# Performance work log

Hardware: AMD Instinct MI355X
Metric: run time of the kernel (lower is better)

Reference implementation:

```python
import jax, jax.numpy as jnp
import numpy as np

N_BINS = 4  # default meteorological bins: [0,5), [5,25), [25,50), [50,100) mm/h in log1p scale


def setup_inputs() -> dict:
    key = jax.random.key(0)
    k1, k2, k3 = jax.random.split(key, 3)
    shape = (16, 1, 15, 384, 384)
    # y_true in [0, 5) (log1p scale) so that all precipitation bins are populated
    y_true = jax.random.uniform(k1, shape, dtype=jnp.float32) * 5.0
    # y_pred: prediction = truth + noise, stays near truth like a trained model
    y_pred = y_true + 0.5 * jax.random.normal(k2, shape, dtype=jnp.float32)
    return {"y_pred": y_pred, "y_true": y_true}


def reference(y_pred, y_true):
    # bins = log1p([0, 5, 25, 50, 100])
    bins = jnp.log1p(jnp.array([0.0, 5.0, 25.0, 50.0, 100.0], dtype=y_true.dtype))
    yp = y_pred.reshape(-1)
    yt = y_true.reshape(-1)
    # bin index i such that bins[i] <= yt < bins[i+1]; -1 below, N_BINS at/above top
    idx = jnp.digitize(yt, bins) - 1
    valid = (idx >= 0) & (idx < N_BINS)
    seg = jnp.where(valid, idx, N_BINS)  # route out-of-range values to a dump bin
    sq = (yp - yt) ** 2
    sumsq = jax.ops.segment_sum(jnp.where(valid, sq, 0.0), seg, num_segments=N_BINS + 1)[:N_BINS]
    counts = jax.ops.segment_sum(valid.astype(yt.dtype), seg, num_segments=N_BINS + 1)[:N_BINS]
    present = counts > 0
    csafe = jnp.where(present, counts, 1.0)
    mse = sumsq / csafe                              # per-bin MSE (0 for empty bins)
    w = jnp.where(present, 1.0 / csafe, 0.0)         # inverse-frequency weights
    wsum = jnp.sum(w)
    wn = w / jnp.where(wsum > 0, wsum, 1.0)          # normalized over non-empty bins
    weighted_mse = jnp.sum(wn * mse)
    loss = jnp.sqrt(weighted_mse + 1e-8)
    return jnp.where(jnp.any(present), loss, jnp.zeros_like(loss))
```

## Files before the change

kernel.cpp:

```cpp
#include <hip/hip_runtime.h>
#include <math.h>

#define NBINS 4
#define SLOTS 64
#define UNROLL 4


__global__ __launch_bounds__(256) void qrmse_bins(
    const float4* __restrict__ yp4, const float4* __restrict__ yt4,
    const float* __restrict__ yp, const float* __restrict__ yt,
    float* __restrict__ g_ss, unsigned int* __restrict__ g_cnt,
    int n4, int n)
{
    const float B1 = 1.7917594909667969f;
    const float B2 = 3.2580965518951416f;
    const float B3 = 3.9318256378173828f;
    const float B4 = 4.6151204109191895f;

    float ss0 = 0.f, ss1 = 0.f, ss2 = 0.f, ss3 = 0.f;
    unsigned int c0 = 0, c1 = 0, c2 = 0, c3 = 0;

    const int base = blockIdx.x * (blockDim.x * UNROLL) + threadIdx.x;

    float4 p[UNROLL], t[UNROLL];
#pragma unroll
    for (int k = 0; k < UNROLL; ++k) {
        int idx = base + k * 256;
        if (idx < n4) {
            p[k] = yp4[idx];
            t[k] = yt4[idx];
        } else {
            p[k] = make_float4(0.f, 0.f, 0.f, 0.f);
            t[k] = make_float4(-1.f, -1.f, -1.f, -1.f);
        }
    }

#define ACC(PC, TC)                                          \
    {                                                        \
        float d  = (PC) - (TC);                              \
        float sq = d * d;                                    \
        float tv = (TC);                                     \
        bool b0 = (tv >= 0.f) & (tv < B1);                   \
        bool b1 = (tv >= B1)  & (tv < B2);                   \
        bool b2 = (tv >= B2)  & (tv < B3);                   \
        bool b3 = (tv >= B3)  & (tv < B4);                   \
        ss0 += b0 ? sq : 0.f;  c0 += b0;                     \
        ss1 += b1 ? sq : 0.f;  c1 += b1;                     \
        ss2 += b2 ? sq : 0.f;  c2 += b2;                     \
        ss3 += b3 ? sq : 0.f;  c3 += b3;                     \
    }

#pragma unroll
    for (int k = 0; k < UNROLL; ++k) {
        ACC(p[k].x, t[k].x); ACC(p[k].y, t[k].y);
        ACC(p[k].z, t[k].z); ACC(p[k].w, t[k].w);
    }

    if (blockIdx.x == 0 && threadIdx.x == 0) {
        for (int i = n4 * 4; i < n; ++i) {
            float pp = yp[i];
            float tt = yt[i];
            ACC(pp, tt);
        }
    }
#undef ACC

    for (int off = 32; off > 0; off >>= 1) {
        ss0 += __shfl_down(ss0, off);
        ss1 += __shfl_down(ss1, off);
        ss2 += __shfl_down(ss2, off);
        ss3 += __shfl_down(ss3, off);
        c0  += __shfl_down(c0,  off);
        c1  += __shfl_down(c1,  off);
        c2  += __shfl_down(c2,  off);
        c3  += __shfl_down(c3,  off);
    }

    __shared__ float        s_ss[4][NBINS];
    __shared__ unsigned int s_cnt[4][NBINS];
    const int lane = threadIdx.x & 63;
    const int wave = threadIdx.x >> 6;
    if (lane == 0) {
        s_ss[wave][0] = ss0; s_ss[wave][1] = ss1;
        s_ss[wave][2] = ss2; s_ss[wave][3] = ss3;
        s_cnt[wave][0] = c0; s_cnt[wave][1] = c1;
        s_cnt[wave][2] = c2; s_cnt[wave][3] = c3;
    }
    __syncthreads();

    if (threadIdx.x == 0) {
        const int slot = blockIdx.x & (SLOTS - 1);
#pragma unroll
        for (int b = 0; b < NBINS; ++b) {
            float bs = s_ss[0][b] + s_ss[1][b] + s_ss[2][b] + s_ss[3][b];
            unsigned int bc = s_cnt[0][b] + s_cnt[1][b] + s_cnt[2][b] + s_cnt[3][b];
            atomicAdd(&g_ss[b * SLOTS + slot], bs);
            atomicAdd(&g_cnt[b * SLOTS + slot], bc);
        }
    }
}

__global__ __launch_bounds__(64) void qrmse_final(
    const float* __restrict__ g_ss,
    const unsigned int* __restrict__ g_cnt,
    float* __restrict__ out)
{
    const int lane = threadIdx.x;
    float ssb[NBINS];
    unsigned int cb[NBINS];
#pragma unroll
    for (int b = 0; b < NBINS; ++b) {
        ssb[b] = g_ss[b * SLOTS + lane];
        cb[b]  = g_cnt[b * SLOTS + lane];
    }
    for (int off = 32; off > 0; off >>= 1) {
#pragma unroll
        for (int b = 0; b < NBINS; ++b) {
            ssb[b] += __shfl_down(ssb[b], off);
            cb[b]  += __shfl_down(cb[b],  off);
        }
    }
    if (lane == 0) {
        float wsum = 0.f;
        float mse[NBINS], w[NBINS];
        bool any = false;
#pragma unroll
        for (int b = 0; b < NBINS; ++b) {
            bool present = (cb[b] > 0);
            any |= present;
            float csafe = present ? (float)cb[b] : 1.0f;
            mse[b] = ssb[b] / csafe;
            w[b] = present ? (1.0f / csafe) : 0.0f;
            wsum += w[b];
        }
        float denom = (wsum > 0.f) ? wsum : 1.0f;
        float wmse = 0.f;
#pragma unroll
        for (int b = 0; b < NBINS; ++b) wmse += (w[b] / denom) * mse[b];
        out[0] = any ? sqrtf(wmse + 1e-8f) : 0.0f;
    }
}

extern "C" void kernel_launch(void* const* d_in, const int* in_sizes, int n_in,
                              void* d_out, int out_size, void* d_ws, size_t ws_size,
                              hipStream_t stream) {
    const float* yp = (const float*)d_in[0];
    const float* yt = (const float*)d_in[1];
    float* out = (float*)d_out;

    float* g_ss = (float*)d_ws;
    unsigned int* g_cnt = (unsigned int*)d_ws + NBINS * SLOTS;

    int n = in_sizes[0];
    int n4 = n / 4;

    hipMemsetAsync(d_ws, 0, 2 * NBINS * SLOTS * sizeof(float), stream);

    const int block = 256;
    const int per_block = block * UNROLL;
    const int grid = (n4 + per_block - 1) / per_block;
    qrmse_bins<<<grid, block, 0, stream>>>(
        (const float4*)yp, (const float4*)yt, yp, yt, g_ss, g_cnt, n4, n);
    qrmse_final<<<1, 64, 0, stream>>>(g_ss, g_cnt, out);
}
```

Baseline: 291.2 us.

## Use fixed-grid persistent blocks with double-buffered tile loads

Replaces the one-shot grid (one block per 1024 float4s, tens of thousands of blocks) with a fixed grid of 2048 blocks. Each block walks a contiguous range of 512-float4 tiles and software-pipelines the work: the next tile's loads are issued before the current tile is accumulated, with sched_barriers to keep that order. This is meant to cut block launch overhead and the number of atomics, and to keep more loads in flight per thread. It adds a remainder path run by block 0 and depends on the compiler honouring the scheduling barriers.

```diff
diff --git a/kernel.cpp b/kernel.cpp
--- a/kernel.cpp
+++ b/kernel.cpp
@@ -3,14 +3,15 @@
 
 #define NBINS 4
 #define SLOTS 64
-#define UNROLL 4
-
+
+
+#define TILE_F4 512
 
 __global__ __launch_bounds__(256) void qrmse_bins(
     const float4* __restrict__ yp4, const float4* __restrict__ yt4,
     const float* __restrict__ yp, const float* __restrict__ yt,
     float* __restrict__ g_ss, unsigned int* __restrict__ g_cnt,
-    int n4, int n)
+    int n4, int n, int total_tiles)
 {
     const float B1 = 1.7917594909667969f;
     const float B2 = 3.2580965518951416f;
@@ -19,21 +20,6 @@
 
     float ss0 = 0.f, ss1 = 0.f, ss2 = 0.f, ss3 = 0.f;
     unsigned int c0 = 0, c1 = 0, c2 = 0, c3 = 0;
-
-    const int base = blockIdx.x * (blockDim.x * UNROLL) + threadIdx.x;
-
-    float4 p[UNROLL], t[UNROLL];
-#pragma unroll
-    for (int k = 0; k < UNROLL; ++k) {
-        int idx = base + k * 256;
-        if (idx < n4) {
-            p[k] = yp4[idx];
-            t[k] = yt4[idx];
-        } else {
-            p[k] = make_float4(0.f, 0.f, 0.f, 0.f);
-            t[k] = make_float4(-1.f, -1.f, -1.f, -1.f);
-        }
-    }
 
 #define ACC(PC, TC)                                          \
     {                                                        \
@@ -49,20 +35,74 @@
         ss2 += b2 ? sq : 0.f;  c2 += b2;                     \
         ss3 += b3 ? sq : 0.f;  c3 += b3;                     \
     }
-
-#pragma unroll
-    for (int k = 0; k < UNROLL; ++k) {
-        ACC(p[k].x, t[k].x); ACC(p[k].y, t[k].y);
-        ACC(p[k].z, t[k].z); ACC(p[k].w, t[k].w);
-    }
-
-    if (blockIdx.x == 0 && threadIdx.x == 0) {
-        for (int i = n4 * 4; i < n; ++i) {
-            float pp = yp[i];
-            float tt = yt[i];
-            ACC(pp, tt);
-        }
-    }
+#define ACC4(P0, P1, T0, T1)                                 \
+    {                                                        \
+        ACC(P0.x, T0.x); ACC(P0.y, T0.y);                    \
+        ACC(P0.z, T0.z); ACC(P0.w, T0.w);                    \
+        ACC(P1.x, T1.x); ACC(P1.y, T1.y);                    \
+        ACC(P1.z, T1.z); ACC(P1.w, T1.w);                    \
+    }
+
+    const int tid = threadIdx.x;
+    const int b   = blockIdx.x;
+    const int G   = gridDim.x;
+
+    const int base    = total_tiles / G;
+    const int extra   = total_tiles % G;
+    const int myStart = b * base + (b < extra ? b : extra);
+    const int myCnt   = base + (b < extra ? 1 : 0);
+
+    if (myCnt > 0) {
+        const float4* Pp = yp4 + myStart * TILE_F4 + tid;
+        const float4* Tp = yt4 + myStart * TILE_F4 + tid;
+
+        float4 pa0, pa1, ta0, ta1;
+        float4 pb0, pb1, tb0, tb1;
+
+        pa0 = Pp[0]; pa1 = Pp[256];
+        ta0 = Tp[0]; ta1 = Tp[256];
+
+        int it = 1;
+        for (; it + 1 < myCnt; it += 2) {
+            Pp += TILE_F4; Tp += TILE_F4;
+            pb0 = Pp[0]; pb1 = Pp[256];
+            tb0 = Tp[0]; tb1 = Tp[256];
+            __builtin_amdgcn_sched_barrier(0);
+            ACC4(pa0, pa1, ta0, ta1);
+
+            Pp += TILE_F4; Tp += TILE_F4;
+            pa0 = Pp[0]; pa1 = Pp[256];
+            ta0 = Tp[0]; ta1 = Tp[256];
+            __builtin_amdgcn_sched_barrier(0);
+            ACC4(pb0, pb1, tb0, tb1);
+        }
+        if (it < myCnt) {
+            Pp += TILE_F4; Tp += TILE_F4;
+            pb0 = Pp[0]; pb1 = Pp[256];
+            tb0 = Tp[0]; tb1 = Tp[256];
+            __builtin_amdgcn_sched_barrier(0);
+            ACC4(pa0, pa1, ta0, ta1);
+            ACC4(pb0, pb1, tb0, tb1);
+        } else {
+            ACC4(pa0, pa1, ta0, ta1);
+        }
+    }
+
+    if (b == 0) {
+        for (int i = total_tiles * TILE_F4 + tid; i < n4; i += 256) {
+            float4 p = yp4[i];
+            float4 t = yt4[i];
+            ACC(p.x, t.x); ACC(p.y, t.y); ACC(p.z, t.z); ACC(p.w, t.w);
+        }
+        if (tid == 0) {
+            for (int i = n4 * 4; i < n; ++i) {
+                float pp = yp[i];
+                float tt = yt[i];
+                ACC(pp, tt);
+            }
+        }
+    }
+#undef ACC4
 #undef ACC
 
     for (int off = 32; off > 0; off >>= 1) {
@@ -78,8 +118,8 @@
 
     __shared__ float        s_ss[4][NBINS];
     __shared__ unsigned int s_cnt[4][NBINS];
-    const int lane = threadIdx.x & 63;
-    const int wave = threadIdx.x >> 6;
+    const int lane = tid & 63;
+    const int wave = tid >> 6;
     if (lane == 0) {
         s_ss[wave][0] = ss0; s_ss[wave][1] = ss1;
         s_ss[wave][2] = ss2; s_ss[wave][3] = ss3;
@@ -88,14 +128,14 @@
     }
     __syncthreads();
 
-    if (threadIdx.x == 0) {
-        const int slot = blockIdx.x & (SLOTS - 1);
-#pragma unroll
-        for (int b = 0; b < NBINS; ++b) {
-            float bs = s_ss[0][b] + s_ss[1][b] + s_ss[2][b] + s_ss[3][b];
-            unsigned int bc = s_cnt[0][b] + s_cnt[1][b] + s_cnt[2][b] + s_cnt[3][b];
-            atomicAdd(&g_ss[b * SLOTS + slot], bs);
-            atomicAdd(&g_cnt[b * SLOTS + slot], bc);
+    if (tid == 0) {
+        const int slot = b & (SLOTS - 1);
+#pragma unroll
+        for (int bin = 0; bin < NBINS; ++bin) {
+            float bs = s_ss[0][bin] + s_ss[1][bin] + s_ss[2][bin] + s_ss[3][bin];
+            unsigned int bc = s_cnt[0][bin] + s_cnt[1][bin] + s_cnt[2][bin] + s_cnt[3][bin];
+            atomicAdd(&g_ss[bin * SLOTS + slot], bs);
+            atomicAdd(&g_cnt[bin * SLOTS + slot], bc);
         }
     }
 }
@@ -151,15 +191,16 @@
     float* g_ss = (float*)d_ws;
     unsigned int* g_cnt = (unsigned int*)d_ws + NBINS * SLOTS;
 
-    int n = in_sizes[0];
+    int n  = in_sizes[0];
     int n4 = n / 4;
+    int total_tiles = n4 / TILE_F4;
 
     hipMemsetAsync(d_ws, 0, 2 * NBINS * SLOTS * sizeof(float), stream);
 
     const int block = 256;
-    const int per_block = block * UNROLL;
-    const int grid = (n4 + per_block - 1) / per_block;
+    const int grid  = 2048;
     qrmse_bins<<<grid, block, 0, stream>>>(
-        (const float4*)yp, (const float4*)yt, yp, yt, g_ss, g_cnt, n4, n);
+        (const float4*)yp, (const float4*)yt, yp, yt, g_ss, g_cnt,
+        n4, n, total_tiles);
     qrmse_final<<<1, 64, 0, stream>>>(g_ss, g_cnt, out);
 }
```

New measurement: 296.8 us. About the same (+1.9%).
